# Kernel optimization log

Hardware: AMD Instinct MI355X
Metric: run time of the kernel (lower is better)

## Reference

```python
import jax
import jax.numpy as jnp
import numpy as np

B, L, D = 4, 1024, 1024
N, K, V = 8, 64, 64
KC = 4  # short conv kernel


def _causal_dwconv_silu(x, w):
    """Depthwise causal conv1d + SiLU. x: (B, L, C), w: (C, KC) -> (B, L, C)."""
    C = w.shape[0]
    y = jax.lax.conv_general_dilated(
        jnp.transpose(x, (0, 2, 1)),        # (B, C, L)
        w[:, None, :],                       # (C, 1, KC)
        window_strides=(1,),
        padding=[(w.shape[1] - 1, 0)],       # causal: left pad only
        feature_group_count=C,
        dimension_numbers=('NCH', 'OIH', 'NCH'))
    return jax.nn.silu(jnp.transpose(y, (0, 2, 1)))


def setup_inputs() -> dict:
    key = jax.random.key(0)
    ks = jax.random.split(key, 12)
    s = 1.0 / np.sqrt(D)
    x = jax.random.normal(ks[0], (B, L, D), dtype=jnp.float32)
    Wq = jax.random.normal(ks[1], (D, N * K), dtype=jnp.float32) * s
    Wk = jax.random.normal(ks[2], (D, N * K), dtype=jnp.float32) * s
    Wv = jax.random.normal(ks[3], (D, N * V), dtype=jnp.float32) * s
    Wf = jax.random.normal(ks[4], (D, N), dtype=jnp.float32) * s
    bf = jnp.zeros((N,), dtype=jnp.float32)
    cw_q = jax.random.normal(ks[5], (N * K, KC), dtype=jnp.float32) * 0.5
    cw_k = jax.random.normal(ks[6], (N * K, KC), dtype=jnp.float32) * 0.5
    cw_v = jax.random.normal(ks[7], (N * V, KC), dtype=jnp.float32) * 0.5
    # transition matrix: identity init (paper) + small noise so grads are non-trivial
    W = jnp.broadcast_to(jnp.eye(V, dtype=jnp.float32), (N, V, V)) \
        + 0.02 * jax.random.normal(ks[8], (N, V, V), dtype=jnp.float32)
    Wo = jax.random.normal(ks[9], (N * V, D), dtype=jnp.float32) * (1.0 / np.sqrt(N * V))
    return {"x": x, "Wq": Wq, "Wk": Wk, "Wv": Wv, "Wf": Wf, "bf": bf,
            "cw_q": cw_q, "cw_k": cw_k, "cw_v": cw_v, "W": W, "Wo": Wo}


def reference(x, Wq, Wk, Wv, Wf, bf, cw_q, cw_k, cw_v, W, Wo):
    Bx, Lx, _ = x.shape
    q = _causal_dwconv_silu(x @ Wq, cw_q)          # (B, L, N*K)
    k = _causal_dwconv_silu(x @ Wk, cw_k)          # (B, L, N*K)
    v = _causal_dwconv_silu(x @ Wv, cw_v)          # (B, L, N*V)
    f = jax.nn.sigmoid(x @ Wf + bf)                # (B, L, N)
    q = q.reshape(Bx, Lx, N, K)
    k = k.reshape(Bx, Lx, N, K)
    v = v.reshape(Bx, Lx, N, V)
    kv = k[..., :, None] * v[..., None, :]         # (B, L, N, K, V)

    H0 = jnp.zeros((Bx, N, K, V), dtype=q.dtype)

    def step(H, inp):
        kv_t, f_t, q_t = inp                       # (B,N,K,V), (B,N), (B,N,K)
        cand = jnp.tanh(jnp.einsum('bnkv,nvw->bnkw', H, W) + kv_t)
        g = f_t[..., None, None]
        H = g * H + (1.0 - g) * cand
        y_t = jnp.einsum('bnk,bnkv->bnv', q_t, H)  # (B, N, V)
        return H, y_t

    xs = (jnp.moveaxis(kv, 1, 0),                  # (L, B, N, K, V)
          jnp.moveaxis(f, 1, 0),                   # (L, B, N)
          jnp.moveaxis(q, 1, 0))                   # (L, B, N, K)
    H_final, ys = jax.lax.scan(step, H0, xs)
    y = jnp.moveaxis(ys, 0, 1).reshape(Bx, Lx, N * V)
    out = y @ Wo                                   # (B, L, D)
    return out, H_final
```

## Files before the change

kernel.cpp:

```cpp
#include <hip/hip_runtime.h>
#include <hip/hip_bf16.h>

typedef __attribute__((ext_vector_type(4))) float f32x4;
typedef __attribute__((ext_vector_type(8))) short short8;
typedef __attribute__((ext_vector_type(4))) int i32x4;
typedef __attribute__((ext_vector_type(2))) unsigned int u32x2;
typedef __attribute__((ext_vector_type(4))) unsigned short u16x4;

static __device__ __forceinline__ unsigned short f2bf(float f) {
  unsigned u = __builtin_bit_cast(unsigned, f);
  u = u + 0x7FFFu + ((u >> 16) & 1u);
  return (unsigned short)(u >> 16);
}
static __device__ __forceinline__ float bf2f(unsigned short b) {
  unsigned u = ((unsigned)b) << 16;
  return __builtin_bit_cast(float, u);
}
static __device__ __forceinline__ float sigmoidf_fast(float x) {
  return __builtin_amdgcn_rcpf(1.f + __expf(-x));
}
static __device__ __forceinline__ unsigned cvt_pk_bf16(float a, float b) {
  unsigned d;
  asm volatile("v_cvt_pk_bf16_f32 %0, %1, %2" : "=v"(d) : "v"(a), "v"(b));
  return d;
}
static __device__ __forceinline__ float row_sum16(float v) {
  int x;
  x = __builtin_amdgcn_update_dpp(0, __builtin_bit_cast(int, v), 0x111, 0xF, 0xF, true);
  v += __builtin_bit_cast(float, x);
  x = __builtin_amdgcn_update_dpp(0, __builtin_bit_cast(int, v), 0x112, 0xF, 0xF, true);
  v += __builtin_bit_cast(float, x);
  x = __builtin_amdgcn_update_dpp(0, __builtin_bit_cast(int, v), 0x114, 0xF, 0xF, true);
  v += __builtin_bit_cast(float, x);
  x = __builtin_amdgcn_update_dpp(0, __builtin_bit_cast(int, v), 0x118, 0xF, 0xF, true);
  v += __builtin_bit_cast(float, x);
  return v;
}

__global__ void cast_split_kernel(const float* __restrict__ in,
                                  unsigned short* __restrict__ oh,
                                  unsigned short* __restrict__ ol, int n4) {
  int i = blockIdx.x * blockDim.x + threadIdx.x;
  if (i >= n4) return;
  f32x4 v = ((const f32x4*)in)[i];
  u16x4 h, l;
#pragma unroll
  for (int j = 0; j < 4; ++j) {
    unsigned short hb = f2bf(v[j]);
    h[j] = hb;
    l[j] = f2bf(v[j] - bf2f(hb));
  }
  ((u16x4*)oh)[i] = h;
  ((u16x4*)ol)[i] = l;
}

__global__ void tcast_kernel(const float* __restrict__ in,
                             unsigned short* __restrict__ out, int R, int C) {
  int i = blockIdx.x * blockDim.x + threadIdx.x;
  if (i >= R * C) return;
  int r = i / C, c = i % C;
  out[(size_t)c * R + r] = f2bf(in[i]);
}

__global__ void tcast_split_kernel(const float* __restrict__ in,
                                   unsigned short* __restrict__ oh,
                                   unsigned short* __restrict__ ol, int R, int C) {
  int i = blockIdx.x * blockDim.x + threadIdx.x;
  if (i >= R * C) return;
  int r = i / C, c = i % C;
  float v = in[i];
  unsigned short hb = f2bf(v);
  oh[(size_t)c * R + r] = hb;
  ol[(size_t)c * R + r] = f2bf(v - bf2f(hb));
}

__global__ __launch_bounds__(256) void fgate_kernel(const float* __restrict__ x,
                                                    const float* __restrict__ Wf,
                                                    const float* __restrict__ bfv,
                                                    float* __restrict__ fbuf) {
  int wid = (blockIdx.x * blockDim.x + threadIdx.x) >> 6;
  int lane = threadIdx.x & 63;
  const float* xr = x + (size_t)wid * 1024;
  float acc[8] = {0.f, 0.f, 0.f, 0.f, 0.f, 0.f, 0.f, 0.f};
#pragma unroll 4
  for (int it = 0; it < 16; ++it) {
    int d = it * 64 + lane;
    float xv = xr[d];
    f32x4 w0 = *(const f32x4*)(Wf + (size_t)d * 8);
    f32x4 w1 = *(const f32x4*)(Wf + (size_t)d * 8 + 4);
    acc[0] += xv * w0[0]; acc[1] += xv * w0[1];
    acc[2] += xv * w0[2]; acc[3] += xv * w0[3];
    acc[4] += xv * w1[0]; acc[5] += xv * w1[1];
    acc[6] += xv * w1[2]; acc[7] += xv * w1[3];
  }
#pragma unroll
  for (int n = 0; n < 8; ++n) {
#pragma unroll
    for (int m = 1; m < 64; m <<= 1) acc[n] += __shfl_xor(acc[n], m, 64);
  }
  if (lane == 0) {
#pragma unroll
    for (int n = 0; n < 8; ++n)
      fbuf[(size_t)wid * 8 + n] = sigmoidf_fast(acc[n] + bfv[n]);
  }
}

__global__ void conv_silu_kernel(const float* __restrict__ pre,
                                 const float* __restrict__ cwq,
                                 const float* __restrict__ cwk,
                                 const float* __restrict__ cwv,
                                 float* __restrict__ outb) {
  int i = blockIdx.x * blockDim.x + threadIdx.x;
  int which = blockIdx.y;
  const float* cw = (which == 0) ? cwq : (which == 1) ? cwk : cwv;
  const float* p = pre + (size_t)which * 2097152 + i;
  int c = i & 511;
  int l = (i >> 9) & 1023;
  float w0 = cw[c * 4 + 0], w1 = cw[c * 4 + 1], w2 = cw[c * 4 + 2], w3 = cw[c * 4 + 3];
  float acc = w3 * p[0];
  if (l >= 1) acc += w2 * p[-512];
  if (l >= 2) acc += w1 * p[-1024];
  if (l >= 3) acc += w0 * p[-1536];
  outb[(size_t)which * 2097152 + i] = acc * sigmoidf_fast(acc);
}

__global__ __launch_bounds__(256) void gemm_bf16_kernel(
    const unsigned short* __restrict__ A, const unsigned short* __restrict__ Bt,
    float* __restrict__ C, int Kd, int Nd, size_t BtStride, size_t CStride) {
  __shared__ unsigned short Ash[128][40];
  __shared__ unsigned short Bsh[128][40];
  const int tid = threadIdx.x;
  const int wave = tid >> 6, lane = tid & 63;
  const int g = lane >> 4, lr = lane & 15;
  const int m0 = blockIdx.x * 128, n0 = blockIdx.y * 128;
  const unsigned short* Bz = Bt + blockIdx.z * BtStride;
  float* Cz = C + blockIdx.z * CStride;
  const int wm = (wave >> 1) * 64, wn = (wave & 1) * 64;

  f32x4 acc[4][4];
#pragma unroll
  for (int a = 0; a < 4; ++a)
#pragma unroll
    for (int bq = 0; bq < 4; ++bq) acc[a][bq] = (f32x4){0.f, 0.f, 0.f, 0.f};

  for (int k0 = 0; k0 < Kd; k0 += 32) {
#pragma unroll
    for (int it = 0; it < 2; ++it) {
      int cch = tid + 256 * it;
      int r = cch >> 2, cc = cch & 3;
      *(i32x4*)&Ash[r][cc * 8] = *(const i32x4*)(A + (size_t)(m0 + r) * Kd + k0 + cc * 8);
      *(i32x4*)&Bsh[r][cc * 8] = *(const i32x4*)(Bz + (size_t)(n0 + r) * Kd + k0 + cc * 8);
    }
    __syncthreads();
    short8 af[4], bfr[4];
#pragma unroll
    for (int mt = 0; mt < 4; ++mt) af[mt] = *(const short8*)&Ash[wm + mt * 16 + lr][g * 8];
#pragma unroll
    for (int nt = 0; nt < 4; ++nt) bfr[nt] = *(const short8*)&Bsh[wn + nt * 16 + lr][g * 8];
#pragma unroll
    for (int mt = 0; mt < 4; ++mt)
#pragma unroll
      for (int nt = 0; nt < 4; ++nt)
        acc[mt][nt] = __builtin_amdgcn_mfma_f32_16x16x32_bf16(af[mt], bfr[nt], acc[mt][nt], 0, 0, 0);
    __syncthreads();
  }
#pragma unroll
  for (int mt = 0; mt < 4; ++mt)
#pragma unroll
    for (int nt = 0; nt < 4; ++nt)
#pragma unroll
      for (int r = 0; r < 4; ++r) {
        int m = m0 + wm + mt * 16 + g * 4 + r;
        int n = n0 + wn + nt * 16 + lr;
        Cz[(size_t)m * Nd + n] = acc[mt][nt][r];
      }
}

__global__ __launch_bounds__(256) void gemm_split_kernel(
    const unsigned short* __restrict__ Ah, const unsigned short* __restrict__ Al,
    const unsigned short* __restrict__ Bth, const unsigned short* __restrict__ Btl,
    float* __restrict__ C, int Kd, int Nd, size_t BtStride, size_t CStride) {
  __shared__ unsigned short AshH[128][40];
  __shared__ unsigned short AshL[128][40];
  __shared__ unsigned short BshH[128][40];
  __shared__ unsigned short BshL[128][40];
  const int tid = threadIdx.x;
  const int wave = tid >> 6, lane = tid & 63;
  const int g = lane >> 4, lr = lane & 15;
  const int m0 = blockIdx.x * 128, n0 = blockIdx.y * 128;
  const unsigned short* Bzh = Bth + blockIdx.z * BtStride;
  const unsigned short* Bzl = Btl + blockIdx.z * BtStride;
  float* Cz = C + blockIdx.z * CStride;
  const int wm = (wave >> 1) * 64, wn = (wave & 1) * 64;

  f32x4 acc[4][4];
#pragma unroll
  for (int a = 0; a < 4; ++a)
#pragma unroll
    for (int bq = 0; bq < 4; ++bq) acc[a][bq] = (f32x4){0.f, 0.f, 0.f, 0.f};

  for (int k0 = 0; k0 < Kd; k0 += 32) {
#pragma unroll
    for (int it = 0; it < 2; ++it) {
      int cch = tid + 256 * it;
      int r = cch >> 2, cc = cch & 3;
      size_t ao = (size_t)(m0 + r) * Kd + k0 + cc * 8;
      size_t bo = (size_t)(n0 + r) * Kd + k0 + cc * 8;
      *(i32x4*)&AshH[r][cc * 8] = *(const i32x4*)(Ah + ao);
      *(i32x4*)&AshL[r][cc * 8] = *(const i32x4*)(Al + ao);
      *(i32x4*)&BshH[r][cc * 8] = *(const i32x4*)(Bzh + bo);
      *(i32x4*)&BshL[r][cc * 8] = *(const i32x4*)(Bzl + bo);
    }
    __syncthreads();
    short8 afh[4], afl[4], bfh[4], bfl[4];
#pragma unroll
    for (int mt = 0; mt < 4; ++mt) {
      afh[mt] = *(const short8*)&AshH[wm + mt * 16 + lr][g * 8];
      afl[mt] = *(const short8*)&AshL[wm + mt * 16 + lr][g * 8];
    }
#pragma unroll
    for (int nt = 0; nt < 4; ++nt) {
      bfh[nt] = *(const short8*)&BshH[wn + nt * 16 + lr][g * 8];
      bfl[nt] = *(const short8*)&BshL[wn + nt * 16 + lr][g * 8];
    }
#pragma unroll
    for (int mt = 0; mt < 4; ++mt)
#pragma unroll
      for (int nt = 0; nt < 4; ++nt) {
        f32x4 a = acc[mt][nt];
        a = __builtin_amdgcn_mfma_f32_16x16x32_bf16(afl[mt], bfh[nt], a, 0, 0, 0);
        a = __builtin_amdgcn_mfma_f32_16x16x32_bf16(afh[mt], bfl[nt], a, 0, 0, 0);
        a = __builtin_amdgcn_mfma_f32_16x16x32_bf16(afh[mt], bfh[nt], a, 0, 0, 0);
        acc[mt][nt] = a;
      }
    __syncthreads();
  }
#pragma unroll
  for (int mt = 0; mt < 4; ++mt)
#pragma unroll
    for (int nt = 0; nt < 4; ++nt)
#pragma unroll
      for (int r = 0; r < 4; ++r) {
        int m = m0 + wm + mt * 16 + g * 4 + r;
        int n = n0 + wn + nt * 16 + lr;
        Cz[(size_t)m * Nd + n] = acc[mt][nt][r];
      }
}

__global__ __launch_bounds__(256) void scan_kernel(
    const float* __restrict__ qbuf, const float* __restrict__ kbuf,
    const float* __restrict__ vbuf, const float* __restrict__ fbuf,
    const float* __restrict__ W, unsigned short* __restrict__ ypart,
    float* __restrict__ Hout) {
  const int tid = threadIdx.x;
  const int wave = tid >> 6, lane = tid & 63;
  const int g = lane >> 4, lr = lane & 15;
  const int bz = blockIdx.x;
  const int chain = bz >> 2, ks = bz & 3;
  const int b = chain >> 3, n = chain & 7;
  const int swz = (lr & 7) << 4;

  __shared__ unsigned short Hh[2][1024];
  __shared__ unsigned short Hl[2][1024];
  __shared__ float stage[2][16][192];
  __shared__ float fs[2][16];
  __shared__ float yst[16][64];

  for (int i = tid; i < 512; i += 256) {
    ((unsigned*)Hh[0])[i] = 0u;
    ((unsigned*)Hl[0])[i] = 0u;
  }

  const float* Wn = W + (size_t)n * 4096;
  short8 Af[2], Alw[2];
#pragma unroll
  for (int s = 0; s < 2; ++s) {
    int wcol = wave * 16 + lr;
    short8 ah, al;
#pragma unroll
    for (int j = 0; j < 8; ++j) {
      float wv = Wn[(size_t)(s * 32 + g * 8 + j) * 64 + wcol];
      unsigned short hb = f2bf(wv);
      ah[j] = (short)hb;
      al[j] = (short)f2bf(wv - bf2f(hb));
    }
    Af[s] = ah; Alw[s] = al;
  }

  auto stage_chunk = [&](int c, int buf) {
#pragma unroll
    for (int i = 0; i < 3; ++i) {
      int fi = tid + i * 256;
      int st = fi / 48, un = fi - st * 48;
      const float* basep = (un < 16) ? qbuf : (un < 32) ? kbuf : vbuf;
      f32x4 val = *(const f32x4*)(basep + (size_t)(b * 1024 + c * 16 + st) * 512 +
                                  n * 64 + (un & 15) * 4);
      *(f32x4*)&stage[buf][st][un * 4] = val;
    }
    if (tid < 16) fs[buf][tid] = fbuf[(size_t)(b * 1024 + c * 16 + tid) * 8 + n];
  };

  f32x4 HA = (f32x4){0.f, 0.f, 0.f, 0.f};
  int sb = 0, pp = 0;

  stage_chunk(0, 0);
  __syncthreads();

  const f32x4 zf = (f32x4){0.f, 0.f, 0.f, 0.f};
  const int bo0 = (16 * g) ^ swz;
  const int bo1 = (64 + 16 * g) ^ swz;
  const int wo = (32 * wave + 8 * g) ^ swz;
  const float K2L2E = 2.885390081777927f;
  const int kg = ks * 16 + lr;

  for (int c = 0; c < 64; ++c) {
    if (c < 63) stage_chunk(c + 1, sb ^ 1);
    for (int tl = 0; tl < 16; ++tl) {
      const float* srow = &stage[sb][tl][0];

      const char* hrh = (const char*)(Hh[pp] + lr * 64);
      const char* hrl = (const char*)(Hl[pp] + lr * 64);
      short8 Bh0 = *(const short8*)(hrh + bo0);
      short8 Bh1 = *(const short8*)(hrh + bo1);
      short8 Bl0 = *(const short8*)(hrl + bo0);
      short8 Bl1 = *(const short8*)(hrl + bo1);

      f32x4 cX = __builtin_amdgcn_mfma_f32_16x16x32_bf16(Alw[0], Bh0, zf, 0, 0, 0);
      f32x4 cY = __builtin_amdgcn_mfma_f32_16x16x32_bf16(Alw[1], Bh1, zf, 0, 0, 0);
      cX = __builtin_amdgcn_mfma_f32_16x16x32_bf16(Af[0], Bl0, cX, 0, 0, 0);
      cY = __builtin_amdgcn_mfma_f32_16x16x32_bf16(Af[1], Bl1, cY, 0, 0, 0);
      cX = __builtin_amdgcn_mfma_f32_16x16x32_bf16(Af[0], Bh0, cX, 0, 0, 0);
      cY = __builtin_amdgcn_mfma_f32_16x16x32_bf16(Af[1], Bh1, cY, 0, 0, 0);

      float kval = srow[64 + kg];
      f32x4 vv = *(const f32x4*)(srow + 128 + wave * 16 + 4 * g);
      float fc = fs[sb][tl];
      f32x4 a0 = cX + cY;

#pragma unroll
      for (int r = 0; r < 4; ++r) {
        float arg = fmaf(kval, vv[r], a0[r]);
        float cd = fmaf(-2.f, __builtin_amdgcn_rcpf(1.f + __builtin_amdgcn_exp2f(arg * K2L2E)), 1.f);
        HA[r] = fmaf(fc, HA[r] - cd, cd);
      }

      {
        float qs = srow[kg];
        float y0 = row_sum16(qs * HA[0]);
        float y1 = row_sum16(qs * HA[1]);
        float y2 = row_sum16(qs * HA[2]);
        float y3 = row_sum16(qs * HA[3]);
        if (lr == 15)
          *(f32x4*)&yst[tl][wave * 16 + 4 * g] = (f32x4){y0, y1, y2, y3};
      }

      {
        char* hwh = (char*)(Hh[pp ^ 1] + lr * 64);
        char* hwl = (char*)(Hl[pp ^ 1] + lr * 64);
        unsigned ph0 = cvt_pk_bf16(HA[0], HA[1]);
        unsigned ph1 = cvt_pk_bf16(HA[2], HA[3]);
        float r0 = HA[0] - __builtin_bit_cast(float, ph0 << 16);
        float r1 = HA[1] - __builtin_bit_cast(float, ph0 & 0xFFFF0000u);
        float r2 = HA[2] - __builtin_bit_cast(float, ph1 << 16);
        float r3 = HA[3] - __builtin_bit_cast(float, ph1 & 0xFFFF0000u);
        *(u32x2*)(hwh + wo) = (u32x2){ph0, ph1};
        *(u32x2*)(hwl + wo) = (u32x2){cvt_pk_bf16(r0, r1), cvt_pk_bf16(r2, r3)};
      }

      __syncthreads();
      pp ^= 1;
    }

    for (int i = tid; i < 1024; i += 256) {
      int tl2 = i >> 6, w = i & 63;
      ypart[(size_t)ks * 2097152 +
            (size_t)(b * 1024 + c * 16 + tl2) * 512 + n * 64 + w] = f2bf(yst[tl2][w]);
    }
    __syncthreads();
    sb ^= 1;
  }

  float* Ho = Hout + (size_t)(b * 8 + n) * 4096;
  *(f32x4*)&Ho[(size_t)kg * 64 + wave * 16 + g * 4] = HA;
}

__global__ void ysum_kernel(const unsigned short* __restrict__ yp,
                            unsigned short* __restrict__ yb) {
  int i = blockIdx.x * 256 + threadIdx.x;
  u16x4 s0 = ((const u16x4*)yp)[i];
  u16x4 s1 = ((const u16x4*)(yp + 2097152))[i];
  u16x4 s2 = ((const u16x4*)(yp + 2 * 2097152))[i];
  u16x4 s3 = ((const u16x4*)(yp + 3 * 2097152))[i];
  u16x4 o;
#pragma unroll
  for (int j = 0; j < 4; ++j)
    o[j] = f2bf(bf2f(s0[j]) + bf2f(s1[j]) + bf2f(s2[j]) + bf2f(s3[j]));
  ((u16x4*)yb)[i] = o;
}

extern "C" void kernel_launch(void* const* d_in, const int* in_sizes, int n_in,
                              void* d_out, int out_size, void* d_ws, size_t ws_size,
                              hipStream_t stream) {
  const float* x   = (const float*)d_in[0];
  const float* Wq  = (const float*)d_in[1];
  const float* Wk  = (const float*)d_in[2];
  const float* Wv  = (const float*)d_in[3];
  const float* Wf  = (const float*)d_in[4];
  const float* bfv = (const float*)d_in[5];
  const float* cwq = (const float*)d_in[6];
  const float* cwk = (const float*)d_in[7];
  const float* cwv = (const float*)d_in[8];
  const float* W   = (const float*)d_in[9];
  const float* Wo  = (const float*)d_in[10];
  float* outp = (float*)d_out;

  char* ws = (char*)d_ws;
  size_t off = 0;
  auto alloc = [&](size_t bytes) {
    char* pp = ws + off;
    off = (off + bytes + 255) & ~(size_t)255;
    return pp;
  };
  unsigned short* xbh  = (unsigned short*)alloc((size_t)4194304 * 2);
  unsigned short* xbl  = (unsigned short*)alloc((size_t)4194304 * 2);
  unsigned short* wtbh = (unsigned short*)alloc((size_t)3 * 524288 * 2);
  unsigned short* wtbl = (unsigned short*)alloc((size_t)3 * 524288 * 2);
  float* pre  = (float*)alloc((size_t)3 * 2097152 * 4);
  float* qkv  = (float*)alloc((size_t)3 * 2097152 * 4);
  float* fbuf = (float*)alloc((size_t)32768 * 4);
  unsigned short* yb  = (unsigned short*)alloc((size_t)2097152 * 2);
  unsigned short* wot = (unsigned short*)alloc((size_t)524288 * 2);
  unsigned short* ypart = (unsigned short*)pre;

  cast_split_kernel<<<4096, 256, 0, stream>>>(x, xbh, xbl, 1048576);
  tcast_split_kernel<<<2048, 256, 0, stream>>>(Wq, wtbh, wtbl, 1024, 512);
  tcast_split_kernel<<<2048, 256, 0, stream>>>(Wk, wtbh + 524288, wtbl + 524288, 1024, 512);
  tcast_split_kernel<<<2048, 256, 0, stream>>>(Wv, wtbh + 2 * 524288, wtbl + 2 * 524288, 1024, 512);
  fgate_kernel<<<1024, 256, 0, stream>>>(x, Wf, bfv, fbuf);
  dim3 gq(32, 4, 1);
  gemm_bf16_kernel<<<gq, 256, 0, stream>>>(xbh, wtbh, pre, 1024, 512,
                                           (size_t)0, (size_t)0);
  dim3 gkv(32, 4, 2);
  gemm_split_kernel<<<gkv, 256, 0, stream>>>(xbh, xbl, wtbh + 524288, wtbl + 524288,
                                             pre + 2097152, 1024, 512,
                                             (size_t)524288, (size_t)2097152);
  dim3 gc(8192, 3, 1);
  conv_silu_kernel<<<gc, 256, 0, stream>>>(pre, cwq, cwk, cwv, qkv);
  scan_kernel<<<128, 256, 0, stream>>>(qkv, qkv + 2097152, qkv + 2 * 2097152, fbuf, W,
                                       ypart, outp + 4194304);
  ysum_kernel<<<2048, 256, 0, stream>>>(ypart, yb);
  tcast_kernel<<<2048, 256, 0, stream>>>(Wo, wot, 512, 1024);
  dim3 g2(32, 8, 1);
  gemm_bf16_kernel<<<g2, 256, 0, stream>>>(yb, wot, outp, 512, 1024, (size_t)0, (size_t)0);
}
```

Before: 721.4 us.

## Interleave two batch chains per scan block to hide recurrence latency

Each scan workgroup now advances two independent batch recurrences (same head, adjacent batches) in lockstep instead of one, halving the grid from 128 to 64 blocks. The two chains' MFMA, tanh and reduction work is interleaved so one chain's independent instructions can fill the dependency stalls of the other, and one barrier per timestep now covers both chains. The cost is doubled LDS usage and register pressure per block and fewer blocks occupying the GPU, though the serial scan was latency-bound rather than throughput-bound.

```diff
diff --git a/kernel.cpp b/kernel.cpp
--- a/kernel.cpp
+++ b/kernel.cpp
@@ -255,20 +255,19 @@
   const int tid = threadIdx.x;
   const int wave = tid >> 6, lane = tid & 63;
   const int g = lane >> 4, lr = lane & 15;
-  const int bz = blockIdx.x;
-  const int chain = bz >> 2, ks = bz & 3;
-  const int b = chain >> 3, n = chain & 7;
+  const int pi = blockIdx.x >> 2, ks = blockIdx.x & 3;
+  const int n = pi & 7, bp = pi >> 3;
   const int swz = (lr & 7) << 4;
 
-  __shared__ unsigned short Hh[2][1024];
-  __shared__ unsigned short Hl[2][1024];
-  __shared__ float stage[2][16][192];
-  __shared__ float fs[2][16];
-  __shared__ float yst[16][64];
+  __shared__ unsigned short Hh[2][2][1024];
+  __shared__ unsigned short Hl[2][2][1024];
+  __shared__ float stage[2][2][16][192];
+  __shared__ float fs[2][2][16];
+  __shared__ float yst[2][16][64];
 
   for (int i = tid; i < 512; i += 256) {
-    ((unsigned*)Hh[0])[i] = 0u;
-    ((unsigned*)Hl[0])[i] = 0u;
+    ((unsigned*)Hh[0][0])[i] = 0u; ((unsigned*)Hl[0][0])[i] = 0u;
+    ((unsigned*)Hh[1][0])[i] = 0u; ((unsigned*)Hl[1][0])[i] = 0u;
   }
 
   const float* Wn = W + (size_t)n * 4096;
@@ -287,20 +286,26 @@
     Af[s] = ah; Alw[s] = al;
   }
 
-  auto stage_chunk = [&](int c, int buf) {
-#pragma unroll
-    for (int i = 0; i < 3; ++i) {
-      int fi = tid + i * 256;
-      int st = fi / 48, un = fi - st * 48;
-      const float* basep = (un < 16) ? qbuf : (un < 32) ? kbuf : vbuf;
-      f32x4 val = *(const f32x4*)(basep + (size_t)(b * 1024 + c * 16 + st) * 512 +
-                                  n * 64 + (un & 15) * 4);
-      *(f32x4*)&stage[buf][st][un * 4] = val;
-    }
-    if (tid < 16) fs[buf][tid] = fbuf[(size_t)(b * 1024 + c * 16 + tid) * 8 + n];
+  auto stage_chunk = [&](int cc, int buf) {
+#pragma unroll
+    for (int ch = 0; ch < 2; ++ch) {
+      const int bb = bp * 2 + ch;
+#pragma unroll
+      for (int i = 0; i < 3; ++i) {
+        int fi = tid + i * 256;
+        int st = fi / 48, un = fi - st * 48;
+        const float* basep = (un < 16) ? qbuf : (un < 32) ? kbuf : vbuf;
+        f32x4 val = *(const f32x4*)(basep + (size_t)(bb * 1024 + cc * 16 + st) * 512 +
+                                    n * 64 + (un & 15) * 4);
+        *(f32x4*)&stage[ch][buf][st][un * 4] = val;
+      }
+      if (tid < 16)
+        fs[ch][buf][tid] = fbuf[(size_t)(bb * 1024 + cc * 16 + tid) * 8 + n];
+    }
   };
 
-  f32x4 HA = (f32x4){0.f, 0.f, 0.f, 0.f};
+  f32x4 H0 = (f32x4){0.f, 0.f, 0.f, 0.f};
+  f32x4 H1 = (f32x4){0.f, 0.f, 0.f, 0.f};
   int sb = 0, pp = 0;
 
   stage_chunk(0, 0);
@@ -316,72 +321,111 @@
   for (int c = 0; c < 64; ++c) {
     if (c < 63) stage_chunk(c + 1, sb ^ 1);
     for (int tl = 0; tl < 16; ++tl) {
-      const float* srow = &stage[sb][tl][0];
-
-      const char* hrh = (const char*)(Hh[pp] + lr * 64);
-      const char* hrl = (const char*)(Hl[pp] + lr * 64);
-      short8 Bh0 = *(const short8*)(hrh + bo0);
-      short8 Bh1 = *(const short8*)(hrh + bo1);
-      short8 Bl0 = *(const short8*)(hrl + bo0);
-      short8 Bl1 = *(const short8*)(hrl + bo1);
-
-      f32x4 cX = __builtin_amdgcn_mfma_f32_16x16x32_bf16(Alw[0], Bh0, zf, 0, 0, 0);
-      f32x4 cY = __builtin_amdgcn_mfma_f32_16x16x32_bf16(Alw[1], Bh1, zf, 0, 0, 0);
-      cX = __builtin_amdgcn_mfma_f32_16x16x32_bf16(Af[0], Bl0, cX, 0, 0, 0);
-      cY = __builtin_amdgcn_mfma_f32_16x16x32_bf16(Af[1], Bl1, cY, 0, 0, 0);
-      cX = __builtin_amdgcn_mfma_f32_16x16x32_bf16(Af[0], Bh0, cX, 0, 0, 0);
-      cY = __builtin_amdgcn_mfma_f32_16x16x32_bf16(Af[1], Bh1, cY, 0, 0, 0);
-
-      float kval = srow[64 + kg];
-      f32x4 vv = *(const f32x4*)(srow + 128 + wave * 16 + 4 * g);
-      float fc = fs[sb][tl];
-      f32x4 a0 = cX + cY;
+      const float* s0 = &stage[0][sb][tl][0];
+      const float* s1 = &stage[1][sb][tl][0];
+
+      const char* h0h = (const char*)(Hh[0][pp] + lr * 64);
+      const char* h0l = (const char*)(Hl[0][pp] + lr * 64);
+      const char* h1h = (const char*)(Hh[1][pp] + lr * 64);
+      const char* h1l = (const char*)(Hl[1][pp] + lr * 64);
+      short8 Bh0_0 = *(const short8*)(h0h + bo0);
+      short8 Bh1_0 = *(const short8*)(h0h + bo1);
+      short8 Bl0_0 = *(const short8*)(h0l + bo0);
+      short8 Bl1_0 = *(const short8*)(h0l + bo1);
+      short8 Bh0_1 = *(const short8*)(h1h + bo0);
+      short8 Bh1_1 = *(const short8*)(h1h + bo1);
+      short8 Bl0_1 = *(const short8*)(h1l + bo0);
+      short8 Bl1_1 = *(const short8*)(h1l + bo1);
+
+      float kv0 = s0[64 + kg], kv1 = s1[64 + kg];
+      f32x4 vv0 = *(const f32x4*)(s0 + 128 + wave * 16 + 4 * g);
+      f32x4 vv1 = *(const f32x4*)(s1 + 128 + wave * 16 + 4 * g);
+      float fc0 = fs[0][sb][tl], fc1 = fs[1][sb][tl];
+      float qs0 = s0[kg], qs1 = s1[kg];
+
+      f32x4 cX0 = __builtin_amdgcn_mfma_f32_16x16x32_bf16(Alw[0], Bh0_0, zf, 0, 0, 0);
+      f32x4 cX1 = __builtin_amdgcn_mfma_f32_16x16x32_bf16(Alw[0], Bh0_1, zf, 0, 0, 0);
+      f32x4 cY0 = __builtin_amdgcn_mfma_f32_16x16x32_bf16(Alw[1], Bh1_0, zf, 0, 0, 0);
+      f32x4 cY1 = __builtin_amdgcn_mfma_f32_16x16x32_bf16(Alw[1], Bh1_1, zf, 0, 0, 0);
+      cX0 = __builtin_amdgcn_mfma_f32_16x16x32_bf16(Af[0], Bl0_0, cX0, 0, 0, 0);
+      cX1 = __builtin_amdgcn_mfma_f32_16x16x32_bf16(Af[0], Bl0_1, cX1, 0, 0, 0);
+      cY0 = __builtin_amdgcn_mfma_f32_16x16x32_bf16(Af[1], Bl1_0, cY0, 0, 0, 0);
+      cY1 = __builtin_amdgcn_mfma_f32_16x16x32_bf16(Af[1], Bl1_1, cY1, 0, 0, 0);
+      cX0 = __builtin_amdgcn_mfma_f32_16x16x32_bf16(Af[0], Bh0_0, cX0, 0, 0, 0);
+      cX1 = __builtin_amdgcn_mfma_f32_16x16x32_bf16(Af[0], Bh0_1, cX1, 0, 0, 0);
+      cY0 = __builtin_amdgcn_mfma_f32_16x16x32_bf16(Af[1], Bh1_0, cY0, 0, 0, 0);
+      cY1 = __builtin_amdgcn_mfma_f32_16x16x32_bf16(Af[1], Bh1_1, cY1, 0, 0, 0);
+
+      f32x4 a0 = cX0 + cY0;
+      f32x4 a1 = cX1 + cY1;
 
 #pragma unroll
       for (int r = 0; r < 4; ++r) {
-        float arg = fmaf(kval, vv[r], a0[r]);
-        float cd = fmaf(-2.f, __builtin_amdgcn_rcpf(1.f + __builtin_amdgcn_exp2f(arg * K2L2E)), 1.f);
-        HA[r] = fmaf(fc, HA[r] - cd, cd);
+        float g0 = fmaf(kv0, vv0[r], a0[r]);
+        float c0 = fmaf(-2.f, __builtin_amdgcn_rcpf(1.f + __builtin_amdgcn_exp2f(g0 * K2L2E)), 1.f);
+        H0[r] = fmaf(fc0, H0[r] - c0, c0);
+        float g1 = fmaf(kv1, vv1[r], a1[r]);
+        float c1 = fmaf(-2.f, __builtin_amdgcn_rcpf(1.f + __builtin_amdgcn_exp2f(g1 * K2L2E)), 1.f);
+        H1[r] = fmaf(fc1, H1[r] - c1, c1);
       }
 
       {
-        float qs = srow[kg];
-        float y0 = row_sum16(qs * HA[0]);
-        float y1 = row_sum16(qs * HA[1]);
-        float y2 = row_sum16(qs * HA[2]);
-        float y3 = row_sum16(qs * HA[3]);
-        if (lr == 15)
-          *(f32x4*)&yst[tl][wave * 16 + 4 * g] = (f32x4){y0, y1, y2, y3};
+        char* w0h = (char*)(Hh[0][pp ^ 1] + lr * 64);
+        char* w0l = (char*)(Hl[0][pp ^ 1] + lr * 64);
+        unsigned ph0 = cvt_pk_bf16(H0[0], H0[1]);
+        unsigned ph1 = cvt_pk_bf16(H0[2], H0[3]);
+        float r0 = H0[0] - __builtin_bit_cast(float, ph0 << 16);
+        float r1 = H0[1] - __builtin_bit_cast(float, ph0 & 0xFFFF0000u);
+        float r2 = H0[2] - __builtin_bit_cast(float, ph1 << 16);
+        float r3 = H0[3] - __builtin_bit_cast(float, ph1 & 0xFFFF0000u);
+        *(u32x2*)(w0h + wo) = (u32x2){ph0, ph1};
+        *(u32x2*)(w0l + wo) = (u32x2){cvt_pk_bf16(r0, r1), cvt_pk_bf16(r2, r3)};
+        char* w1h = (char*)(Hh[1][pp ^ 1] + lr * 64);
+        char* w1l = (char*)(Hl[1][pp ^ 1] + lr * 64);
+        unsigned qh0 = cvt_pk_bf16(H1[0], H1[1]);
+        unsigned qh1 = cvt_pk_bf16(H1[2], H1[3]);
+        float s0r = H1[0] - __builtin_bit_cast(float, qh0 << 16);
+        float s1r = H1[1] - __builtin_bit_cast(float, qh0 & 0xFFFF0000u);
+        float s2r = H1[2] - __builtin_bit_cast(float, qh1 << 16);
+        float s3r = H1[3] - __builtin_bit_cast(float, qh1 & 0xFFFF0000u);
+        *(u32x2*)(w1h + wo) = (u32x2){qh0, qh1};
+        *(u32x2*)(w1l + wo) = (u32x2){cvt_pk_bf16(s0r, s1r), cvt_pk_bf16(s2r, s3r)};
       }
 
       {
-        char* hwh = (char*)(Hh[pp ^ 1] + lr * 64);
-        char* hwl = (char*)(Hl[pp ^ 1] + lr * 64);
-        unsigned ph0 = cvt_pk_bf16(HA[0], HA[1]);
-        unsigned ph1 = cvt_pk_bf16(HA[2], HA[3]);
-        float r0 = HA[0] - __builtin_bit_cast(float, ph0 << 16);
-        float r1 = HA[1] - __builtin_bit_cast(float, ph0 & 0xFFFF0000u);
-        float r2 = HA[2] - __builtin_bit_cast(float, ph1 << 16);
-        float r3 = HA[3] - __builtin_bit_cast(float, ph1 & 0xFFFF0000u);
-        *(u32x2*)(hwh + wo) = (u32x2){ph0, ph1};
-        *(u32x2*)(hwl + wo) = (u32x2){cvt_pk_bf16(r0, r1), cvt_pk_bf16(r2, r3)};
+        float y00 = row_sum16(qs0 * H0[0]);
+        float y01 = row_sum16(qs0 * H0[1]);
+        float y02 = row_sum16(qs0 * H0[2]);
+        float y03 = row_sum16(qs0 * H0[3]);
+        float y10 = row_sum16(qs1 * H1[0]);
+        float y11 = row_sum16(qs1 * H1[1]);
+        float y12 = row_sum16(qs1 * H1[2]);
+        float y13 = row_sum16(qs1 * H1[3]);
+        if (lr == 15) {
+          *(f32x4*)&yst[0][tl][wave * 16 + 4 * g] = (f32x4){y00, y01, y02, y03};
+          *(f32x4*)&yst[1][tl][wave * 16 + 4 * g] = (f32x4){y10, y11, y12, y13};
+        }
       }
 
       __syncthreads();
       pp ^= 1;
     }
 
-    for (int i = tid; i < 1024; i += 256) {
-      int tl2 = i >> 6, w = i & 63;
+    for (int i = tid; i < 2048; i += 256) {
+      int ch = i >> 10, r = i & 1023;
+      int tl2 = r >> 6, w = r & 63;
+      int bb = bp * 2 + ch;
       ypart[(size_t)ks * 2097152 +
-            (size_t)(b * 1024 + c * 16 + tl2) * 512 + n * 64 + w] = f2bf(yst[tl2][w]);
+            (size_t)(bb * 1024 + c * 16 + tl2) * 512 + n * 64 + w] = f2bf(yst[ch][tl2][w]);
     }
     __syncthreads();
     sb ^= 1;
   }
 
-  float* Ho = Hout + (size_t)(b * 8 + n) * 4096;
-  *(f32x4*)&Ho[(size_t)kg * 64 + wave * 16 + g * 4] = HA;
+  float* Ho0 = Hout + (size_t)((bp * 2 + 0) * 8 + n) * 4096;
+  float* Ho1 = Hout + (size_t)((bp * 2 + 1) * 8 + n) * 4096;
+  *(f32x4*)&Ho0[(size_t)kg * 64 + wave * 16 + g * 4] = H0;
+  *(f32x4*)&Ho1[(size_t)kg * 64 + wave * 16 + g * 4] = H1;
 }
 
 __global__ void ysum_kernel(const unsigned short* __restrict__ yp,
@@ -446,8 +490,8 @@
                                              (size_t)524288, (size_t)2097152);
   dim3 gc(8192, 3, 1);
   conv_silu_kernel<<<gc, 256, 0, stream>>>(pre, cwq, cwk, cwv, qkv);
-  scan_kernel<<<128, 256, 0, stream>>>(qkv, qkv + 2097152, qkv + 2 * 2097152, fbuf, W,
-                                       ypart, outp + 4194304);
+  scan_kernel<<<64, 256, 0, stream>>>(qkv, qkv + 2097152, qkv + 2 * 2097152, fbuf, W,
+                                      ypart, outp + 4194304);
   ysum_kernel<<<2048, 256, 0, stream>>>(ypart, yb);
   tcast_kernel<<<2048, 256, 0, stream>>>(Wo, wot, 512, 1024);
   dim3 g2(32, 8, 1);
```

After: 971.7 us. +34.7%, slower.

## Halve scan block to two waves, each computing two 16-column H tiles

Applied to the files above, without the earlier changes.

The scan kernel drops from four waves to two per block. Each wave now owns two 16-column output tiles of H and issues twice the MFMAs per timestep, reusing the same B fragments loaded from LDS. The aim is a cheaper per-step __syncthreads across fewer waves and more independent MFMA/transcendental work per wave to hide latency in the serial recurrence. The cost is more registers per wave, a longer per-wave critical path each step, and more staging loads per thread.

```diff
diff --git a/kernel.cpp b/kernel.cpp
--- a/kernel.cpp
+++ b/kernel.cpp
@@ -247,7 +247,7 @@
       }
 }
 
-__global__ __launch_bounds__(256) void scan_kernel(
+__global__ __launch_bounds__(128) void scan_kernel(
     const float* __restrict__ qbuf, const float* __restrict__ kbuf,
     const float* __restrict__ vbuf, const float* __restrict__ fbuf,
     const float* __restrict__ W, unsigned short* __restrict__ ypart,
@@ -266,31 +266,33 @@
   __shared__ float fs[2][16];
   __shared__ float yst[16][64];
 
-  for (int i = tid; i < 512; i += 256) {
+  for (int i = tid; i < 512; i += 128) {
     ((unsigned*)Hh[0])[i] = 0u;
     ((unsigned*)Hl[0])[i] = 0u;
   }
 
   const float* Wn = W + (size_t)n * 4096;
-  short8 Af[2], Alw[2];
-#pragma unroll
-  for (int s = 0; s < 2; ++s) {
-    int wcol = wave * 16 + lr;
-    short8 ah, al;
-#pragma unroll
-    for (int j = 0; j < 8; ++j) {
-      float wv = Wn[(size_t)(s * 32 + g * 8 + j) * 64 + wcol];
-      unsigned short hb = f2bf(wv);
-      ah[j] = (short)hb;
-      al[j] = (short)f2bf(wv - bf2f(hb));
-    }
-    Af[s] = ah; Alw[s] = al;
-  }
+  short8 Af[2][2], Alw[2][2];
+#pragma unroll
+  for (int wb = 0; wb < 2; ++wb)
+#pragma unroll
+    for (int s = 0; s < 2; ++s) {
+      int wcol = (wave * 2 + wb) * 16 + lr;
+      short8 ah, al;
+#pragma unroll
+      for (int j = 0; j < 8; ++j) {
+        float wv = Wn[(size_t)(s * 32 + g * 8 + j) * 64 + wcol];
+        unsigned short hb = f2bf(wv);
+        ah[j] = (short)hb;
+        al[j] = (short)f2bf(wv - bf2f(hb));
+      }
+      Af[wb][s] = ah; Alw[wb][s] = al;
+    }
 
   auto stage_chunk = [&](int c, int buf) {
 #pragma unroll
-    for (int i = 0; i < 3; ++i) {
-      int fi = tid + i * 256;
+    for (int i = 0; i < 6; ++i) {
+      int fi = tid + i * 128;
       int st = fi / 48, un = fi - st * 48;
       const float* basep = (un < 16) ? qbuf : (un < 32) ? kbuf : vbuf;
       f32x4 val = *(const f32x4*)(basep + (size_t)(b * 1024 + c * 16 + st) * 512 +
@@ -301,6 +303,7 @@
   };
 
   f32x4 HA = (f32x4){0.f, 0.f, 0.f, 0.f};
+  f32x4 HB = (f32x4){0.f, 0.f, 0.f, 0.f};
   int sb = 0, pp = 0;
 
   stage_chunk(0, 0);
@@ -309,7 +312,8 @@
   const f32x4 zf = (f32x4){0.f, 0.f, 0.f, 0.f};
   const int bo0 = (16 * g) ^ swz;
   const int bo1 = (64 + 16 * g) ^ swz;
-  const int wo = (32 * wave + 8 * g) ^ swz;
+  const int wo0 = (32 * (wave * 2 + 0) + 8 * g) ^ swz;
+  const int wo1 = (32 * (wave * 2 + 1) + 8 * g) ^ swz;
   const float K2L2E = 2.885390081777927f;
   const int kg = ks * 16 + lr;
 
@@ -325,33 +329,36 @@
       short8 Bl0 = *(const short8*)(hrl + bo0);
       short8 Bl1 = *(const short8*)(hrl + bo1);
 
-      f32x4 cX = __builtin_amdgcn_mfma_f32_16x16x32_bf16(Alw[0], Bh0, zf, 0, 0, 0);
-      f32x4 cY = __builtin_amdgcn_mfma_f32_16x16x32_bf16(Alw[1], Bh1, zf, 0, 0, 0);
-      cX = __builtin_amdgcn_mfma_f32_16x16x32_bf16(Af[0], Bl0, cX, 0, 0, 0);
-      cY = __builtin_amdgcn_mfma_f32_16x16x32_bf16(Af[1], Bl1, cY, 0, 0, 0);
-      cX = __builtin_amdgcn_mfma_f32_16x16x32_bf16(Af[0], Bh0, cX, 0, 0, 0);
-      cY = __builtin_amdgcn_mfma_f32_16x16x32_bf16(Af[1], Bh1, cY, 0, 0, 0);
-
       float kval = srow[64 + kg];
-      f32x4 vv = *(const f32x4*)(srow + 128 + wave * 16 + 4 * g);
+      f32x4 vv0 = *(const f32x4*)(srow + 128 + (wave * 2 + 0) * 16 + 4 * g);
+      f32x4 vv1 = *(const f32x4*)(srow + 128 + (wave * 2 + 1) * 16 + 4 * g);
       float fc = fs[sb][tl];
-      f32x4 a0 = cX + cY;
+      float qs = srow[kg];
+
+      f32x4 cX0 = __builtin_amdgcn_mfma_f32_16x16x32_bf16(Alw[0][0], Bh0, zf, 0, 0, 0);
+      f32x4 cX1 = __builtin_amdgcn_mfma_f32_16x16x32_bf16(Alw[1][0], Bh0, zf, 0, 0, 0);
+      f32x4 cY0 = __builtin_amdgcn_mfma_f32_16x16x32_bf16(Alw[0][1], Bh1, zf, 0, 0, 0);
+      f32x4 cY1 = __builtin_amdgcn_mfma_f32_16x16x32_bf16(Alw[1][1], Bh1, zf, 0, 0, 0);
+      cX0 = __builtin_amdgcn_mfma_f32_16x16x32_bf16(Af[0][0], Bl0, cX0, 0, 0, 0);
+      cX1 = __builtin_amdgcn_mfma_f32_16x16x32_bf16(Af[1][0], Bl0, cX1, 0, 0, 0);
+      cY0 = __builtin_amdgcn_mfma_f32_16x16x32_bf16(Af[0][1], Bl1, cY0, 0, 0, 0);
+      cY1 = __builtin_amdgcn_mfma_f32_16x16x32_bf16(Af[1][1], Bl1, cY1, 0, 0, 0);
+      cX0 = __builtin_amdgcn_mfma_f32_16x16x32_bf16(Af[0][0], Bh0, cX0, 0, 0, 0);
+      cX1 = __builtin_amdgcn_mfma_f32_16x16x32_bf16(Af[1][0], Bh0, cX1, 0, 0, 0);
+      cY0 = __builtin_amdgcn_mfma_f32_16x16x32_bf16(Af[0][1], Bh1, cY0, 0, 0, 0);
+      cY1 = __builtin_amdgcn_mfma_f32_16x16x32_bf16(Af[1][1], Bh1, cY1, 0, 0, 0);
+
+      f32x4 a0 = cX0 + cY0;
+      f32x4 a1 = cX1 + cY1;
 
 #pragma unroll
       for (int r = 0; r < 4; ++r) {
-        float arg = fmaf(kval, vv[r], a0[r]);
-        float cd = fmaf(-2.f, __builtin_amdgcn_rcpf(1.f + __builtin_amdgcn_exp2f(arg * K2L2E)), 1.f);
-        HA[r] = fmaf(fc, HA[r] - cd, cd);
-      }
-
-      {
-        float qs = srow[kg];
-        float y0 = row_sum16(qs * HA[0]);
-        float y1 = row_sum16(qs * HA[1]);
-        float y2 = row_sum16(qs * HA[2]);
-        float y3 = row_sum16(qs * HA[3]);
-        if (lr == 15)
-          *(f32x4*)&yst[tl][wave * 16 + 4 * g] = (f32x4){y0, y1, y2, y3};
+        float g0 = fmaf(kval, vv0[r], a0[r]);
+        float c0 = fmaf(-2.f, __builtin_amdgcn_rcpf(1.f + __builtin_amdgcn_exp2f(g0 * K2L2E)), 1.f);
+        HA[r] = fmaf(fc, HA[r] - c0, c0);
+        float g1 = fmaf(kval, vv1[r], a1[r]);
+        float c1 = fmaf(-2.f, __builtin_amdgcn_rcpf(1.f + __builtin_amdgcn_exp2f(g1 * K2L2E)), 1.f);
+        HB[r] = fmaf(fc, HB[r] - c1, c1);
       }
 
       {
@@ -363,15 +370,38 @@
         float r1 = HA[1] - __builtin_bit_cast(float, ph0 & 0xFFFF0000u);
         float r2 = HA[2] - __builtin_bit_cast(float, ph1 << 16);
         float r3 = HA[3] - __builtin_bit_cast(float, ph1 & 0xFFFF0000u);
-        *(u32x2*)(hwh + wo) = (u32x2){ph0, ph1};
-        *(u32x2*)(hwl + wo) = (u32x2){cvt_pk_bf16(r0, r1), cvt_pk_bf16(r2, r3)};
+        *(u32x2*)(hwh + wo0) = (u32x2){ph0, ph1};
+        *(u32x2*)(hwl + wo0) = (u32x2){cvt_pk_bf16(r0, r1), cvt_pk_bf16(r2, r3)};
+        unsigned qh0 = cvt_pk_bf16(HB[0], HB[1]);
+        unsigned qh1 = cvt_pk_bf16(HB[2], HB[3]);
+        float s0 = HB[0] - __builtin_bit_cast(float, qh0 << 16);
+        float s1 = HB[1] - __builtin_bit_cast(float, qh0 & 0xFFFF0000u);
+        float s2 = HB[2] - __builtin_bit_cast(float, qh1 << 16);
+        float s3 = HB[3] - __builtin_bit_cast(float, qh1 & 0xFFFF0000u);
+        *(u32x2*)(hwh + wo1) = (u32x2){qh0, qh1};
+        *(u32x2*)(hwl + wo1) = (u32x2){cvt_pk_bf16(s0, s1), cvt_pk_bf16(s2, s3)};
+      }
+
+      {
+        float y0 = row_sum16(qs * HA[0]);
+        float y1 = row_sum16(qs * HA[1]);
+        float y2 = row_sum16(qs * HA[2]);
+        float y3 = row_sum16(qs * HA[3]);
+        float y4 = row_sum16(qs * HB[0]);
+        float y5 = row_sum16(qs * HB[1]);
+        float y6 = row_sum16(qs * HB[2]);
+        float y7 = row_sum16(qs * HB[3]);
+        if (lr == 15) {
+          *(f32x4*)&yst[tl][(wave * 2 + 0) * 16 + 4 * g] = (f32x4){y0, y1, y2, y3};
+          *(f32x4*)&yst[tl][(wave * 2 + 1) * 16 + 4 * g] = (f32x4){y4, y5, y6, y7};
+        }
       }
 
       __syncthreads();
       pp ^= 1;
     }
 
-    for (int i = tid; i < 1024; i += 256) {
+    for (int i = tid; i < 1024; i += 128) {
       int tl2 = i >> 6, w = i & 63;
       ypart[(size_t)ks * 2097152 +
             (size_t)(b * 1024 + c * 16 + tl2) * 512 + n * 64 + w] = f2bf(yst[tl2][w]);
@@ -381,7 +411,8 @@
   }
 
   float* Ho = Hout + (size_t)(b * 8 + n) * 4096;
-  *(f32x4*)&Ho[(size_t)kg * 64 + wave * 16 + g * 4] = HA;
+  *(f32x4*)&Ho[(size_t)kg * 64 + (wave * 2 + 0) * 16 + g * 4] = HA;
+  *(f32x4*)&Ho[(size_t)kg * 64 + (wave * 2 + 1) * 16 + g * 4] = HB;
 }
 
 __global__ void ysum_kernel(const unsigned short* __restrict__ yp,
@@ -446,7 +477,7 @@
                                              (size_t)524288, (size_t)2097152);
   dim3 gc(8192, 3, 1);
   conv_silu_kernel<<<gc, 256, 0, stream>>>(pre, cwq, cwk, cwv, qkv);
-  scan_kernel<<<128, 256, 0, stream>>>(qkv, qkv + 2097152, qkv + 2 * 2097152, fbuf, W,
+  scan_kernel<<<128, 128, 0, stream>>>(qkv, qkv + 2097152, qkv + 2 * 2097152, fbuf, W,
                                        ypart, outp + 4194304);
   ysum_kernel<<<2048, 256, 0, stream>>>(ypart, yb);
   tcast_kernel<<<2048, 256, 0, stream>>>(Wo, wot, 512, 1024);
```

Result: slower. 895.8 us (+24.2%).

## Run scan recurrence in one wavefront per chain and drop per-step barriers

Applied to the files above, without the earlier changes.

The scan kernel drops from four waves per block to a single 64-lane wave. That wave computes all four 16-column tiles of the state update, holding 4x the W fragments and state registers. This removes the __syncthreads after every timestep and after each chunk, since LDS ordering within one wave suffices. The price is four times the serial MFMA, transcendental and reduction work per wave on the critical path, more register pressure, and a single wave per CU to hide global staging loads. The y partial writeback also changes to packed 32-bit stores.

```diff
diff --git a/kernel.cpp b/kernel.cpp
--- a/kernel.cpp
+++ b/kernel.cpp
@@ -247,13 +247,12 @@
       }
 }
 
-__global__ __launch_bounds__(256) void scan_kernel(
+__global__ __launch_bounds__(64) void scan_kernel(
     const float* __restrict__ qbuf, const float* __restrict__ kbuf,
     const float* __restrict__ vbuf, const float* __restrict__ fbuf,
     const float* __restrict__ W, unsigned short* __restrict__ ypart,
     float* __restrict__ Hout) {
-  const int tid = threadIdx.x;
-  const int wave = tid >> 6, lane = tid & 63;
+  const int lane = threadIdx.x & 63;
   const int g = lane >> 4, lr = lane & 15;
   const int bz = blockIdx.x;
   const int chain = bz >> 2, ks = bz & 3;
@@ -266,50 +265,55 @@
   __shared__ float fs[2][16];
   __shared__ float yst[16][64];
 
-  for (int i = tid; i < 512; i += 256) {
+  for (int i = lane; i < 512; i += 64) {
     ((unsigned*)Hh[0])[i] = 0u;
     ((unsigned*)Hl[0])[i] = 0u;
   }
 
   const float* Wn = W + (size_t)n * 4096;
-  short8 Af[2], Alw[2];
-#pragma unroll
-  for (int s = 0; s < 2; ++s) {
-    int wcol = wave * 16 + lr;
-    short8 ah, al;
-#pragma unroll
-    for (int j = 0; j < 8; ++j) {
-      float wv = Wn[(size_t)(s * 32 + g * 8 + j) * 64 + wcol];
-      unsigned short hb = f2bf(wv);
-      ah[j] = (short)hb;
-      al[j] = (short)f2bf(wv - bf2f(hb));
-    }
-    Af[s] = ah; Alw[s] = al;
-  }
+  short8 Af[4][2], Alw[4][2];
+#pragma unroll
+  for (int t = 0; t < 4; ++t)
+#pragma unroll
+    for (int s = 0; s < 2; ++s) {
+      int wcol = t * 16 + lr;
+      short8 ah, al;
+#pragma unroll
+      for (int j = 0; j < 8; ++j) {
+        float wv = Wn[(size_t)(s * 32 + g * 8 + j) * 64 + wcol];
+        unsigned short hb = f2bf(wv);
+        ah[j] = (short)hb;
+        al[j] = (short)f2bf(wv - bf2f(hb));
+      }
+      Af[t][s] = ah; Alw[t][s] = al;
+    }
 
   auto stage_chunk = [&](int c, int buf) {
 #pragma unroll
-    for (int i = 0; i < 3; ++i) {
-      int fi = tid + i * 256;
+    for (int i = 0; i < 12; ++i) {
+      int fi = lane + i * 64;
       int st = fi / 48, un = fi - st * 48;
       const float* basep = (un < 16) ? qbuf : (un < 32) ? kbuf : vbuf;
       f32x4 val = *(const f32x4*)(basep + (size_t)(b * 1024 + c * 16 + st) * 512 +
                                   n * 64 + (un & 15) * 4);
       *(f32x4*)&stage[buf][st][un * 4] = val;
     }
-    if (tid < 16) fs[buf][tid] = fbuf[(size_t)(b * 1024 + c * 16 + tid) * 8 + n];
+    if (lane < 16) fs[buf][lane] = fbuf[(size_t)(b * 1024 + c * 16 + lane) * 8 + n];
   };
 
-  f32x4 HA = (f32x4){0.f, 0.f, 0.f, 0.f};
+  f32x4 H[4];
+#pragma unroll
+  for (int t = 0; t < 4; ++t) H[t] = (f32x4){0.f, 0.f, 0.f, 0.f};
   int sb = 0, pp = 0;
 
   stage_chunk(0, 0);
-  __syncthreads();
 
   const f32x4 zf = (f32x4){0.f, 0.f, 0.f, 0.f};
   const int bo0 = (16 * g) ^ swz;
   const int bo1 = (64 + 16 * g) ^ swz;
-  const int wo = (32 * wave + 8 * g) ^ swz;
+  int wo[4];
+#pragma unroll
+  for (int t = 0; t < 4; ++t) wo[t] = (32 * t + 8 * g) ^ swz;
   const float K2L2E = 2.885390081777927f;
   const int kg = ks * 16 + lr;
 
@@ -325,63 +329,86 @@
       short8 Bl0 = *(const short8*)(hrl + bo0);
       short8 Bl1 = *(const short8*)(hrl + bo1);
 
-      f32x4 cX = __builtin_amdgcn_mfma_f32_16x16x32_bf16(Alw[0], Bh0, zf, 0, 0, 0);
-      f32x4 cY = __builtin_amdgcn_mfma_f32_16x16x32_bf16(Alw[1], Bh1, zf, 0, 0, 0);
-      cX = __builtin_amdgcn_mfma_f32_16x16x32_bf16(Af[0], Bl0, cX, 0, 0, 0);
-      cY = __builtin_amdgcn_mfma_f32_16x16x32_bf16(Af[1], Bl1, cY, 0, 0, 0);
-      cX = __builtin_amdgcn_mfma_f32_16x16x32_bf16(Af[0], Bh0, cX, 0, 0, 0);
-      cY = __builtin_amdgcn_mfma_f32_16x16x32_bf16(Af[1], Bh1, cY, 0, 0, 0);
-
       float kval = srow[64 + kg];
-      f32x4 vv = *(const f32x4*)(srow + 128 + wave * 16 + 4 * g);
       float fc = fs[sb][tl];
-      f32x4 a0 = cX + cY;
-
-#pragma unroll
-      for (int r = 0; r < 4; ++r) {
-        float arg = fmaf(kval, vv[r], a0[r]);
-        float cd = fmaf(-2.f, __builtin_amdgcn_rcpf(1.f + __builtin_amdgcn_exp2f(arg * K2L2E)), 1.f);
-        HA[r] = fmaf(fc, HA[r] - cd, cd);
-      }
-
-      {
-        float qs = srow[kg];
-        float y0 = row_sum16(qs * HA[0]);
-        float y1 = row_sum16(qs * HA[1]);
-        float y2 = row_sum16(qs * HA[2]);
-        float y3 = row_sum16(qs * HA[3]);
-        if (lr == 15)
-          *(f32x4*)&yst[tl][wave * 16 + 4 * g] = (f32x4){y0, y1, y2, y3};
+      float qs = srow[kg];
+      f32x4 vv[4];
+#pragma unroll
+      for (int t = 0; t < 4; ++t)
+        vv[t] = *(const f32x4*)(srow + 128 + t * 16 + 4 * g);
+
+      f32x4 cX[4], cY[4];
+#pragma unroll
+      for (int t = 0; t < 4; ++t) {
+        cX[t] = __builtin_amdgcn_mfma_f32_16x16x32_bf16(Alw[t][0], Bh0, zf, 0, 0, 0);
+        cY[t] = __builtin_amdgcn_mfma_f32_16x16x32_bf16(Alw[t][1], Bh1, zf, 0, 0, 0);
+      }
+#pragma unroll
+      for (int t = 0; t < 4; ++t) {
+        cX[t] = __builtin_amdgcn_mfma_f32_16x16x32_bf16(Af[t][0], Bl0, cX[t], 0, 0, 0);
+        cY[t] = __builtin_amdgcn_mfma_f32_16x16x32_bf16(Af[t][1], Bl1, cY[t], 0, 0, 0);
+      }
+#pragma unroll
+      for (int t = 0; t < 4; ++t) {
+        cX[t] = __builtin_amdgcn_mfma_f32_16x16x32_bf16(Af[t][0], Bh0, cX[t], 0, 0, 0);
+        cY[t] = __builtin_amdgcn_mfma_f32_16x16x32_bf16(Af[t][1], Bh1, cY[t], 0, 0, 0);
+      }
+
+#pragma unroll
+      for (int t = 0; t < 4; ++t) {
+        f32x4 a = cX[t] + cY[t];
+#pragma unroll
+        for (int r = 0; r < 4; ++r) {
+          float arg = fmaf(kval, vv[t][r], a[r]);
+          float cd = fmaf(-2.f, __builtin_amdgcn_rcpf(1.f + __builtin_amdgcn_exp2f(arg * K2L2E)), 1.f);
+          H[t][r] = fmaf(fc, H[t][r] - cd, cd);
+        }
       }
 
       {
         char* hwh = (char*)(Hh[pp ^ 1] + lr * 64);
         char* hwl = (char*)(Hl[pp ^ 1] + lr * 64);
-        unsigned ph0 = cvt_pk_bf16(HA[0], HA[1]);
-        unsigned ph1 = cvt_pk_bf16(HA[2], HA[3]);
-        float r0 = HA[0] - __builtin_bit_cast(float, ph0 << 16);
-        float r1 = HA[1] - __builtin_bit_cast(float, ph0 & 0xFFFF0000u);
-        float r2 = HA[2] - __builtin_bit_cast(float, ph1 << 16);
-        float r3 = HA[3] - __builtin_bit_cast(float, ph1 & 0xFFFF0000u);
-        *(u32x2*)(hwh + wo) = (u32x2){ph0, ph1};
-        *(u32x2*)(hwl + wo) = (u32x2){cvt_pk_bf16(r0, r1), cvt_pk_bf16(r2, r3)};
-      }
-
-      __syncthreads();
+#pragma unroll
+        for (int t = 0; t < 4; ++t) {
+          unsigned ph0 = cvt_pk_bf16(H[t][0], H[t][1]);
+          unsigned ph1 = cvt_pk_bf16(H[t][2], H[t][3]);
+          float r0 = H[t][0] - __builtin_bit_cast(float, ph0 << 16);
+          float r1 = H[t][1] - __builtin_bit_cast(float, ph0 & 0xFFFF0000u);
+          float r2 = H[t][2] - __builtin_bit_cast(float, ph1 << 16);
+          float r3 = H[t][3] - __builtin_bit_cast(float, ph1 & 0xFFFF0000u);
+          *(u32x2*)(hwh + wo[t]) = (u32x2){ph0, ph1};
+          *(u32x2*)(hwl + wo[t]) = (u32x2){cvt_pk_bf16(r0, r1), cvt_pk_bf16(r2, r3)};
+        }
+      }
+
+#pragma unroll
+      for (int t = 0; t < 4; ++t) {
+        float y0 = row_sum16(qs * H[t][0]);
+        float y1 = row_sum16(qs * H[t][1]);
+        float y2 = row_sum16(qs * H[t][2]);
+        float y3 = row_sum16(qs * H[t][3]);
+        if (lr == 15)
+          *(f32x4*)&yst[tl][t * 16 + 4 * g] = (f32x4){y0, y1, y2, y3};
+      }
+
       pp ^= 1;
     }
 
-    for (int i = tid; i < 1024; i += 256) {
-      int tl2 = i >> 6, w = i & 63;
-      ypart[(size_t)ks * 2097152 +
-            (size_t)(b * 1024 + c * 16 + tl2) * 512 + n * 64 + w] = f2bf(yst[tl2][w]);
-    }
-    __syncthreads();
+#pragma unroll
+    for (int i = 0; i < 8; ++i) {
+      int j = i * 64 + lane;
+      int tl2 = j >> 5, w = (j & 31) * 2;
+      unsigned val = (unsigned)f2bf(yst[tl2][w]) | ((unsigned)f2bf(yst[tl2][w + 1]) << 16);
+      *(unsigned*)(ypart + (size_t)ks * 2097152 +
+                   (size_t)(b * 1024 + c * 16 + tl2) * 512 + n * 64 + w) = val;
+    }
     sb ^= 1;
   }
 
   float* Ho = Hout + (size_t)(b * 8 + n) * 4096;
-  *(f32x4*)&Ho[(size_t)kg * 64 + wave * 16 + g * 4] = HA;
+#pragma unroll
+  for (int t = 0; t < 4; ++t)
+    *(f32x4*)&Ho[(size_t)kg * 64 + t * 16 + g * 4] = H[t];
 }
 
 __global__ void ysum_kernel(const unsigned short* __restrict__ yp,
@@ -446,8 +473,8 @@
                                              (size_t)524288, (size_t)2097152);
   dim3 gc(8192, 3, 1);
   conv_silu_kernel<<<gc, 256, 0, stream>>>(pre, cwq, cwk, cwv, qkv);
-  scan_kernel<<<128, 256, 0, stream>>>(qkv, qkv + 2097152, qkv + 2 * 2097152, fbuf, W,
-                                       ypart, outp + 4194304);
+  scan_kernel<<<128, 64, 0, stream>>>(qkv, qkv + 2097152, qkv + 2 * 2097152, fbuf, W,
+                                      ypart, outp + 4194304);
   ysum_kernel<<<2048, 256, 0, stream>>>(ypart, yb);
   tcast_kernel<<<2048, 256, 0, stream>>>(Wo, wot, 512, 1024);
   dim3 g2(32, 8, 1);
```

After: 1.512 ms. 110% more time.
